# Performance work log

Measured on AMD Instinct MI355X. Metric: run time of the kernel, lower is better.

## Reference

```python
import jax, jax.numpy as jnp
import numpy as np
from jax import lax

B, H, W = 4, 64, 64
D_MODEL, D_INNER, D_STATE, DT_RANK, K = 128, 256, 16, 8, 4


def _ln(x, g, b, eps=1e-5):
    m = x.mean(-1, keepdims=True)
    v = x.var(-1, keepdims=True)
    return (x - m) * lax.rsqrt(v + eps) * g + b


def _conv(x, w, groups=1):
    return lax.conv_general_dilated(x, w, (1, 1), 'SAME', feature_group_count=groups,
                                    dimension_numbers=('NCHW', 'OIHW', 'NCHW'))


def _bn(x, g, b, m, v, eps=1e-5):  # BatchNorm2d eval mode
    s = g * lax.rsqrt(v + eps)
    return x * s[None, :, None, None] + (b - m * s)[None, :, None, None]


def _resblock(x, w1, g1, b1, m1, v1, w2, g2, b2, m2, v2):
    out = jax.nn.relu(_bn(_conv(x, w1), g1, b1, m1, v1))
    out = _bn(_conv(out, w2), g2, b2, m2, v2)
    return jax.nn.relu(out + x)


def _selective_scan(u, delta, A, Bs, Cs, Ds):
    # u, delta: (B,K,D,L); Bs, Cs: (B,K,N,L); A: (K,D,N); Ds: (K,D)
    ins = (jnp.moveaxis(u, -1, 0), jnp.moveaxis(delta, -1, 0),
           jnp.moveaxis(Bs, -1, 0), jnp.moveaxis(Cs, -1, 0))
    h0 = jnp.zeros(u.shape[:3] + (A.shape[-1],), u.dtype)  # (B,K,D,N)
    def step(h, inp):
        u_t, d_t, B_t, C_t = inp
        h = jnp.exp(d_t[..., None] * A) * h + (d_t * u_t)[..., None] * B_t[:, :, None, :]
        return h, jnp.einsum('bkdn,bkn->bkd', h, C_t)
    _, ys = lax.scan(step, h0, ins)
    return jnp.moveaxis(ys, 0, -1) + u * Ds[None, :, :, None]


def _ss2d(x, in_proj_w, dw_w, dw_b, x_proj_w, dt_proj_w, dt_proj_b, A_logs, Ds,
          onorm_g, onorm_b, out_proj_w):
    b, h, w, _ = x.shape
    L = h * w
    xp, z = jnp.split(x @ in_proj_w.T, 2, axis=-1)
    xp = jnp.transpose(xp, (0, 3, 1, 2))  # (B,Dn,H,W)
    xp = jax.nn.silu(_conv(xp, dw_w, groups=D_INNER) + dw_b[None, :, None, None])
    # cross scan: row-major, col-major, and their reverses (K=4)
    x0 = xp.reshape(b, D_INNER, L)
    x1 = jnp.swapaxes(xp, 2, 3).reshape(b, D_INNER, L)
    xs = jnp.stack([x0, x1, x0[..., ::-1], x1[..., ::-1]], axis=1)  # (B,K,Dn,L)
    x_dbl = jnp.einsum('bkdl,kcd->bkcl', xs, x_proj_w)
    dts, Bm, Cm = jnp.split(x_dbl, [DT_RANK, DT_RANK + D_STATE], axis=2)
    delta = jax.nn.softplus(jnp.einsum('bkrl,kdr->bkdl', dts, dt_proj_w)
                            + dt_proj_b[None, :, :, None])
    ys = _selective_scan(xs, delta, -jnp.exp(A_logs), Bm, Cm, Ds)
    # cross merge
    ys = ys[:, 0:2] + ys[:, 2:4][..., ::-1]
    y = ys[:, 0] + jnp.swapaxes(ys[:, 1].reshape(b, D_INNER, w, h), 2, 3).reshape(b, D_INNER, L)
    y = _ln(jnp.transpose(y.reshape(b, D_INNER, h, w), (0, 2, 3, 1)), onorm_g, onorm_b)
    return (y * jax.nn.silu(z)) @ out_proj_w.T


def setup_inputs():
    key = jax.random.key(0)
    ks = iter(jax.random.split(key, 48))
    f32 = jnp.float32
    nrm = lambda shp, s: jax.random.normal(next(ks), shp, f32) * s
    d, dn, n, r = D_MODEL, D_INNER, D_STATE, DT_RANK
    return dict(
        x1=jax.random.normal(next(ks), (B, d, H, W), f32),
        x2=jax.random.normal(next(ks), (B, d, H, W), f32),
        conv_in_w=nrm((d, d), d ** -0.5), conv_in_b=nrm((d,), 0.01),
        ln1_g=jnp.ones(d, f32), ln1_b=jnp.zeros(d, f32),
        in_proj_w=nrm((2 * dn, d), d ** -0.5),
        dw_w=nrm((dn, 1, 3, 3), 1.0 / 3.0), dw_b=nrm((dn,), 0.01),
        x_proj_w=nrm((K, r + 2 * n, dn), dn ** -0.5),
        dt_proj_w=nrm((K, dn, r), r ** -0.5),
        dt_proj_b=jax.random.uniform(next(ks), (K, dn), f32, 0.0, 0.1),
        A_logs=jnp.tile(jnp.log(jnp.arange(1, n + 1, dtype=f32)), (K, dn, 1)),
        Ds=jnp.ones((K, dn), f32),
        onorm_g=jnp.ones(dn, f32), onorm_b=jnp.zeros(dn, f32),
        out_proj_w=nrm((d, dn), dn ** -0.5),
        ln2_g=jnp.ones(d, f32), ln2_b=jnp.zeros(d, f32),
        mlp_w1=nrm((4 * d, d), d ** -0.5), mlp_b1=jnp.zeros(4 * d, f32),
        mlp_w2=nrm((d, 4 * d), (4 * d) ** -0.5), mlp_b2=jnp.zeros(d, f32),
        rb1_w=nrm((d, d, 3, 3), (9 * d) ** -0.5),
        bn1_g=jnp.ones(d, f32), bn1_b=jnp.zeros(d, f32), bn1_m=nrm((d,), 0.1), bn1_v=jnp.ones(d, f32),
        rb2_w=nrm((d, d, 3, 3), (9 * d) ** -0.5),
        bn2_g=jnp.ones(d, f32), bn2_b=jnp.zeros(d, f32), bn2_m=nrm((d,), 0.1), bn2_v=jnp.ones(d, f32),
    )


def reference(x1, x2, conv_in_w, conv_in_b, ln1_g, ln1_b, in_proj_w, dw_w, dw_b,
              x_proj_w, dt_proj_w, dt_proj_b, A_logs, Ds, onorm_g, onorm_b, out_proj_w,
              ln2_g, ln2_b, mlp_w1, mlp_b1, mlp_w2, mlp_b2,
              rb1_w, bn1_g, bn1_b, bn1_m, bn1_v, rb2_w, bn2_g, bn2_b, bn2_m, bn2_v):
    b, c, h, w = x1.shape
    # strided interleave along width: ct[..., ::2]=x1, ct[..., 1::2]=x2
    ct = jnp.stack([x1, x2], axis=-1).reshape(b, c, h, 2 * w)
    x = jnp.einsum('bchw,oc->bohw', ct, conv_in_w) + conv_in_b[None, :, None, None]
    x = jnp.transpose(x, (0, 2, 3, 1))  # (B,H,2W,C) channel-last
    # VSSBlock (drop_path is identity at eval)
    x = x + _ss2d(_ln(x, ln1_g, ln1_b), in_proj_w, dw_w, dw_b, x_proj_w,
                  dt_proj_w, dt_proj_b, A_logs, Ds, onorm_g, onorm_b, out_proj_w)
    hm = _ln(x, ln2_g, ln2_b)
    x = x + (jax.nn.gelu(hm @ mlp_w1.T + mlp_b1, approximate=False) @ mlp_w2.T + mlp_b2)
    xf = jnp.transpose(x, (0, 3, 1, 2))
    x1f = xf[:, :, :, 0::2]
    x2f = xf[:, :, :, 1::2]
    rb = lambda t: _resblock(t, rb1_w, bn1_g, bn1_b, bn1_m, bn1_v,
                             rb2_w, bn2_g, bn2_b, bn2_m, bn2_v)
    return (rb(x1f), rb(x2f))
```

## Files before the change

kernel.cpp:

```cpp
#include <hip/hip_runtime.h>
#include <math.h>

#define BB 4
#define CM 128
#define DI 256
#define NS 16
#define RK 8
#define KD 4
#define HH 64
#define WW 128
#define LL 8192
#define NC 8
#define CH 1024

typedef unsigned short ushortt;
typedef unsigned int uintt;
typedef __attribute__((ext_vector_type(8))) __bf16 bf16x8;
typedef __attribute__((ext_vector_type(4))) float f32x4;

__device__ __forceinline__ void lds_fence(){
  asm volatile("" ::: "memory");
}

__device__ __forceinline__ float sigmoidf_(float x){ return 1.f/(1.f+__expf(-x)); }
__device__ __forceinline__ float siluf_(float x){ return x*sigmoidf_(x); }
__device__ __forceinline__ float softplusf_(float x){
  float r = __logf(1.f + __expf(x));
  return (x > 20.f) ? x : r;
}
__device__ __forceinline__ float geluf_(float x){ return 0.5f*x*(1.f+erff(x*0.70710678118654752f)); }
__device__ __forceinline__ ushortt f2bf(float f){
  uintt u = __float_as_uint(f);
  uintt r = (u + 0x7fffu + ((u>>16)&1u)) >> 16;
  return (ushortt)r;
}
__device__ __forceinline__ float bf2f(ushortt s){
  return __uint_as_float(((uintt)s)<<16);
}
template<int CTRL>
__device__ __forceinline__ float dppadd(float x){
  int r = __builtin_amdgcn_update_dpp(0, __float_as_int(x), CTRL, 0xF, 0xF, true);
  return x + __int_as_float(r);
}
__device__ __forceinline__ float rowsum16(float x){
  x = dppadd<0x121>(x);
  x = dppadd<0x122>(x);
  x = dppadd<0x124>(x);
  x = dppadd<0x128>(x);
  return x;
}
__device__ __forceinline__ float waveReduceSum(float v){
  for (int o=32;o>0;o>>=1) v += __shfl_xor(v,o,64);
  return v;
}

__global__ void k_wall(const float* __restrict__ cw_s, ushortt* __restrict__ cw_d,
                       const float* __restrict__ ip_s, ushortt* __restrict__ ip_d,
                       const float* __restrict__ op_s, ushortt* __restrict__ op_d,
                       const float* __restrict__ m1_s, ushortt* __restrict__ m1_d,
                       const float* __restrict__ m2_s, ushortt* __restrict__ m2_d,
                       const float* __restrict__ r1_s, ushortt* __restrict__ r1_d,
                       const float* __restrict__ r2_s, ushortt* __restrict__ r2_d,
                       const float* __restrict__ dw_s, float* __restrict__ dw_d,
                       const float* __restrict__ xp_s, ushortt* __restrict__ xp_d){
  int i = blockIdx.x*256 + threadIdx.x;
  if (i < 16384){ cw_d[i] = f2bf(cw_s[i]); return; }
  i -= 16384;
  if (i < 65536){ ip_d[i] = f2bf(ip_s[i]); return; }
  i -= 65536;
  if (i < 32768){ op_d[i] = f2bf(op_s[i]); return; }
  i -= 32768;
  if (i < 65536){ m1_d[i] = f2bf(m1_s[i]); return; }
  i -= 65536;
  if (i < 65536){ m2_d[i] = f2bf(m2_s[i]); return; }
  i -= 65536;
  if (i < 147456){ int ci=i&127, co=(i>>7)&127, tap=i>>14;
    r1_d[i]=f2bf(r1_s[(size_t)(co*128+ci)*9+tap]); return; }
  i -= 147456;
  if (i < 147456){ int ci=i&127, co=(i>>7)&127, tap=i>>14;
    r2_d[i]=f2bf(r2_s[(size_t)(co*128+ci)*9+tap]); return; }
  i -= 147456;
  if (i < 2304){ int d = i & 255, tap = i >> 8;
    dw_d[i] = dw_s[d*9 + tap]; return; }
  i -= 2304;
  if (i < 81920){
    int d = i & 255, row = i >> 8;
    float v; int lo;
    if (row < 64){
      int rr = row & 31; int k = rr>>3, c = rr&7;
      v = xp_s[((size_t)(k*40+c))*256 + d];
      lo = (row >= 32);
    } else {
      int rr = row - 64; int q = rr>>6, s = rr&63;
      int j = s & 31;
      v = xp_s[((size_t)(q*40+8+j))*256 + d];
      lo = (s >= 32);
    }
    xp_d[i] = lo ? f2bf(v - bf2f(f2bf(v))) : f2bf(v);
  }
}

__global__ void k_build_ct2(const float* __restrict__ x1, const float* __restrict__ x2,
                            ushortt* __restrict__ CT){
  __shared__ ushortt Tl[64][136];
  int tid = threadIdx.x;
  int p0 = (blockIdx.x & 127) * 64;
  int b  = blockIdx.x >> 7;
  int j = tid & 63;
  int p = p0 + j; int hh = p>>7, ww = p&127, w2 = ww>>1;
  const float* src = (ww&1) ? x2 : x1;
  const float* sp = src + ((size_t)b*128*64 + hh)*64 + w2;
  for (int c0 = tid>>6; c0 < 128; c0 += 4)
    Tl[j][c0] = f2bf(sp[(size_t)c0*4096]);
  __syncthreads();
  int c = tid & 127; int rh = tid >> 7;
  for (int r = rh; r < 64; r += 2)
    CT[((size_t)b*LL + p0 + r)*128 + c] = Tl[r][c];
}

template<int EPI, int NF>
__global__ void k_mgemm(const ushortt* __restrict__ A, const ushortt* __restrict__ W,
                        const float* __restrict__ bias, const float* __restrict__ resid,
                        float* __restrict__ C, ushortt* __restrict__ C2,
                        ushortt* __restrict__ Pp, float* __restrict__ Rp, int N, int K){
  int n0 = blockIdx.x*(NF*16), m0 = blockIdx.y*64;
  int wv = threadIdx.x>>6, l = threadIdx.x&63;
  int ar = l&15, kg = l>>4;
  int mw = m0 + wv*16;
  f32x4 acc[NF];
#pragma unroll
  for (int i=0;i<NF;i++){ acc[i][0]=0.f; acc[i][1]=0.f; acc[i][2]=0.f; acc[i][3]=0.f; }
  const ushortt* Ap = A + (size_t)(mw+ar)*K + kg*8;
  const ushortt* Wp = W + (size_t)(n0+ar)*K + kg*8;
  for (int k0=0; k0<K; k0+=32){
    bf16x8 af = *(const bf16x8*)(Ap + k0);
#pragma unroll
    for (int nf=0; nf<NF; ++nf){
      bf16x8 bfv = *(const bf16x8*)(Wp + (size_t)nf*16*K + k0);
      acc[nf] = __builtin_amdgcn_mfma_f32_16x16x32_bf16(af, bfv, acc[nf], 0,0,0);
    }
  }
#pragma unroll
  for (int nf=0;nf<NF;nf++){
    int n = n0 + nf*16 + ar;
#pragma unroll
    for (int r=0;r<4;r++){
      int m = mw + kg*4 + r;
      float v = acc[nf][r];
      if (EPI==2){
        v += bias[n];
        C2[(size_t)m*512 + n] = f2bf(geluf_(v));
      } else if (EPI==3){
        if (n < 256) Pp[(size_t)m*256 + n] = f2bf(v);
        else         C2[(size_t)m*256 + (n-256)] = f2bf(v);
      } else {
        v += bias[n];
        v += resid[(size_t)m*128 + n];
        int bq = m >> 13; int pq = m & 8191; int yq = pq >> 7; int wq = pq & 127;
        int im = (wq&1)*4 + bq; int xq = wq>>1;
        Pp[(((size_t)im*66 + yq+1)*66 + xq+1)*128 + n] = f2bf(v);
        Rp[(((size_t)im*64 + yq)*64 + xq)*128 + n] = v;
      }
    }
  }
}

template<int RES>
__global__ void k_mgemmln(const ushortt* __restrict__ A, const ushortt* __restrict__ W,
                          const float* __restrict__ bias, float* __restrict__ X,
                          const float* __restrict__ g, const float* __restrict__ bt,
                          ushortt* __restrict__ O, int K){
  int m0 = blockIdx.x*64;
  int wv = threadIdx.x>>6, l = threadIdx.x&63;
  int ar = l&15, kg = l>>4;
  int mw = m0 + wv*16;
  f32x4 acc[8];
#pragma unroll
  for (int i=0;i<8;i++){ acc[i][0]=0.f; acc[i][1]=0.f; acc[i][2]=0.f; acc[i][3]=0.f; }
  const ushortt* Ap = A + (size_t)(mw+ar)*K + kg*8;
  const ushortt* Wp = W + (size_t)ar*K + kg*8;
  for (int k0=0; k0<K; k0+=32){
    bf16x8 af = *(const bf16x8*)(Ap + k0);
#pragma unroll
    for (int nf=0; nf<8; ++nf){
      bf16x8 bfv = *(const bf16x8*)(Wp + (size_t)nf*16*K + k0);
      acc[nf] = __builtin_amdgcn_mfma_f32_16x16x32_bf16(af, bfv, acc[nf], 0,0,0);
    }
  }
  float vv[8][4];
  float s[4] = {0,0,0,0}, s2[4] = {0,0,0,0};
#pragma unroll
  for (int nf=0;nf<8;nf++){
    int n = nf*16 + ar;
    float bv = bias ? bias[n] : 0.f;
#pragma unroll
    for (int r=0;r<4;r++){
      int m = mw + kg*4 + r;
      float v = acc[nf][r] + bv;
      if (RES) v += X[(size_t)m*128 + n];
      X[(size_t)m*128 + n] = v;
      vv[nf][r] = v;
      s[r] += v; s2[r] += v*v;
    }
  }
  float mn[4], rs[4];
#pragma unroll
  for (int r=0;r<4;r++){
    float S  = rowsum16(s[r]);
    float S2 = rowsum16(s2[r]);
    float mean = S*(1.f/128.f);
    float var  = S2*(1.f/128.f) - mean*mean;
    mn[r] = mean; rs[r] = rsqrtf(var + 1e-5f);
  }
#pragma unroll
  for (int nf=0;nf<8;nf++){
    int n = nf*16 + ar;
    float gv = g[n], bv = bt[n];
#pragma unroll
    for (int r=0;r<4;r++){
      int m = mw + kg*4 + r;
      O[(size_t)m*128 + n] = f2bf((vv[nf][r]-mn[r])*rs[r]*gv + bv);
    }
  }
}

__global__ void k_dwconv(const ushortt* __restrict__ Xp, const float* __restrict__ dwt,
                         const float* __restrict__ bias, ushortt* __restrict__ O){
  __shared__ ushortt S[3][18][256];
  int tid = threadIdx.x;
  int ws0 = blockIdx.x*16;
  int hh  = blockIdx.y;
  int b   = blockIdx.z;
  for (int v = tid; v < 1728; v += 256){
    int d0 = (v & 31)*8;
    int r  = v >> 5;
    int dy = r/18, j = r - dy*18;
    int yy = hh + dy - 1, xx = ws0 + j - 1;
    uint4 val = make_uint4(0,0,0,0);
    if (yy>=0 && yy<HH && xx>=0 && xx<WW)
      val = *(const uint4*)(Xp + ((size_t)b*LL + yy*WW + xx)*256 + d0);
    *(uint4*)(&S[dy][j][d0]) = val;
  }
  __syncthreads();
  int d = tid;
  float w[9];
#pragma unroll
  for (int t=0;t<9;t++) w[t] = dwt[t*256+d];
  float bv = bias[d];
  float a0=bf2f(S[0][0][d]), a1=bf2f(S[1][0][d]), a2=bf2f(S[2][0][d]);
  float b0=bf2f(S[0][1][d]), b1=bf2f(S[1][1][d]), b2=bf2f(S[2][1][d]);
  for (int j=0;j<16;j++){
    float c0=bf2f(S[0][j+2][d]), c1=bf2f(S[1][j+2][d]), c2=bf2f(S[2][j+2][d]);
    float acc = bv;
    acc += a0*w[0] + b0*w[1] + c0*w[2];
    acc += a1*w[3] + b1*w[4] + c1*w[5];
    acc += a2*w[6] + b2*w[7] + c2*w[8];
    O[((size_t)b*LL + hh*WW + ws0 + j)*256 + d] = f2bf(siluf_(acc));
    a0=b0; a1=b1; a2=b2; b0=c0; b1=c1; b2=c2;
  }
}

__global__ void k_xtm(const ushortt* __restrict__ Xpab, ushortt* __restrict__ Xpt0,
                      ushortt* __restrict__ Xpt1){
  __shared__ ushortt Tl[64][68];
  int zb = blockIdx.z; int b = zb >> 1; int mode = zb & 1;
  int d0 = blockIdx.y*64;
  int di = threadIdx.x&63, q = threadIdx.x>>6;
  if (mode == 0){
    int p0 = blockIdx.x*64;
    for (int k2=0;k2<16;k2++){ int pi = q*16 + k2;
      Tl[pi][di] = Xpab[((size_t)b*LL + p0+pi)*256 + d0+di]; }
    __syncthreads();
    for (int k2=0;k2<16;k2++){ int dr = q*16 + k2;
      Xpt0[((size_t)(b*256 + d0+dr))*LL + p0+di] = Tl[di][dr]; }
  } else {
    int ww = blockIdx.x;
    for (int k2=0;k2<16;k2++){ int hh = q*16 + k2;
      Tl[hh][di] = Xpab[((size_t)b*LL + hh*128 + ww)*256 + d0+di]; }
    __syncthreads();
    for (int k2=0;k2<16;k2++){ int dr = q*16 + k2;
      Xpt1[((size_t)(b*256 + d0+dr))*LL + ww*64 + di] = Tl[di][dr]; }
  }
}

__global__ void k_xproj(const ushortt* __restrict__ A, const ushortt* __restrict__ W,
                        float* __restrict__ DBCf, char* __restrict__ BCsb){
  int n0 = blockIdx.x*64, m0 = blockIdx.y*64;
  int wv = threadIdx.x>>6, l = threadIdx.x&63;
  int ar = l&15, kg = l>>4;
  int mw = m0 + wv*16;
  f32x4 acc[4];
#pragma unroll
  for (int i=0;i<4;i++){ acc[i][0]=0.f; acc[i][1]=0.f; acc[i][2]=0.f; acc[i][3]=0.f; }
  const ushortt* Ap = A + (size_t)(mw+ar)*256 + kg*8;
  const ushortt* Wp = W + (size_t)(n0+ar)*256 + kg*8;
#pragma unroll
  for (int k0=0; k0<256; k0+=32){
    bf16x8 af = *(const bf16x8*)(Ap + k0);
#pragma unroll
    for (int nf=0; nf<4; ++nf){
      bf16x8 bfv = *(const bf16x8*)(Wp + (size_t)nf*16*256 + k0);
      acc[nf] = __builtin_amdgcn_mfma_f32_16x16x32_bf16(af, bfv, acc[nf], 0,0,0);
    }
  }
  if (blockIdx.x == 0){
#pragma unroll
    for (int nf=0;nf<2;nf++){
      int n = nf*16 + ar;
      int kq = n>>3, cq = n&7;
#pragma unroll
      for (int r=0;r<4;r++){
        int m = mw + kg*4 + r;
        int b = m >> 13, p = m & 8191;
        int hh = p>>7, ww = p&127;
        int tc = (ww<<6)|hh;
        int t = (kq==0)? p : (kq==1)? tc : (kq==2)? (8191-p) : (8191-tc);
        int bk = b*KD + kq;
        DBCf[((size_t)bk*LL + t)*8 + cq] = acc[nf][r] + acc[nf+2][r];
      }
    }
  } else {
    int q = blockIdx.x - 1;
#pragma unroll
    for (int nf=0;nf<2;nf++){
      int st = ar;
      int hi = (nf==1) ? 2 : 0;
#pragma unroll
      for (int r=0;r<4;r++){
        int m = mw + kg*4 + r;
        int b = m >> 13, p = m & 8191;
        int hh = p>>7, ww = p&127;
        int tc = (ww<<6)|hh;
        int t = (q==0)? p : (q==1)? tc : (q==2)? (8191-p) : (8191-tc);
        int bk = b*KD + q;
        float v = acc[nf][r] + acc[nf+2][r];
        size_t a = ((((size_t)bk*512 + (t>>4))*16 + st)*16 + (t&15))*4 + hi;
        *(ushortt*)(BCsb + a) = f2bf(v);
      }
    }
  }
}

__global__ __launch_bounds__(128) void k_scanM(const char* __restrict__ DBCb,
                        const uintt* __restrict__ BCs,
                        const ushortt* __restrict__ Xpt0, const ushortt* __restrict__ Xpt1,
                        const float* __restrict__ dtw_all, const float* __restrict__ dtb_all,
                        const float* __restrict__ A_logs,
                        float* __restrict__ Hbuf, float* __restrict__ Ssum,
                        ushortt* __restrict__ Y0, ushortt* __restrict__ Y1,
                        ushortt* __restrict__ Y2, ushortt* __restrict__ Y3){
  __shared__ float2 sdd[8][16];
  __shared__ float yt[8*328];
  int tid = threadIdx.x;
  int grp = tid >> 4, lane = tid & 15;
  float* ytg = yt + grp*328;
  int gid = blockIdx.x*8 + grp;
  int c = gid & (NC-1);
  int bkd = gid / NC;
  int b = bkd >> 10, k = (bkd>>8)&3, d = bkd & 255;
  int kd = k*256+d;
  int bk = b*KD + k;
  float dtw[8];
  { const float4* w4 = (const float4*)(dtw_all + (size_t)kd*8);
    float4 w0 = w4[0], w1 = w4[1];
    dtw[0]=w0.x; dtw[1]=w0.y; dtw[2]=w0.z; dtw[3]=w0.w;
    dtw[4]=w1.x; dtw[5]=w1.y; dtw[6]=w1.z; dtw[7]=w1.w; }
  float dtb  = dtb_all[kd];
  float Aval = -__expf(A_logs[(size_t)kd*16+lane]);
  const char* dbc = DBCb + (size_t)bk*LL*32;
  const uintt* bcb = BCs + ((size_t)bk*512 + (c*CH>>4))*256;
  const ushortt* Up = ((k&1)?Xpt1:Xpt0) + ((size_t)(b*256+d))*LL;
  ushortt* Yk = (k==0?Y0 : k==1?Y1 : k==2?Y2 : Y3) + ((size_t)b*256 + d)*LL;
  float h = 0.f, Sacc = 0.f;
  int t0 = c*CH;
  const char* row0 = dbc + (size_t)(t0+lane)*32;
  float4 q0 = *(const float4*)row0;
  float4 q1 = *(const float4*)(row0+16);
  ushortt ur = Up[(k<2) ? (t0+lane) : (LL-1-(t0+lane))];
  for (int blk=0; blk<CH/16; ++blk){
    int tb = t0 + blk*16;
    int tme = tb + lane;
    const uint4* bcp = (const uint4*)(bcb + ((size_t)blk*16 + lane)*16);
    uint4 w0 = bcp[0], w1 = bcp[1], w2 = bcp[2], w3 = bcp[3];
    float4 c0 = q0, c1 = q1; ushortt cu = ur;
    if (blk+1 < CH/16){
      const char* rn = dbc + (size_t)(tme+16)*32;
      q0 = *(const float4*)rn;
      q1 = *(const float4*)(rn+16);
      ur = Up[(k<2) ? (tme+16) : (LL-1-(tme+16))];
    }
    float dsum = dtb + c0.x*dtw[0] + c0.y*dtw[1] + c0.z*dtw[2] + c0.w*dtw[3]
                     + c1.x*dtw[4] + c1.y*dtw[5] + c1.z*dtw[6] + c1.w*dtw[7];
    float delta = softplusf_(dsum);
    Sacc += delta;
    float u = bf2f(cu);
    sdd[grp][lane] = make_float2(delta, delta*u);
    lds_fence();
    uintt wd[16] = {w0.x,w0.y,w0.z,w0.w, w1.x,w1.y,w1.z,w1.w,
                    w2.x,w2.y,w2.z,w2.w, w3.x,w3.y,w3.z,w3.w};
#pragma unroll
    for (int i=0;i<16;i++){
      float2 dd = sdd[grp][i];
      uintt w = wd[i];
      float Bn = __uint_as_float(w<<16);
      float Cn = __uint_as_float(w & 0xffff0000u);
      float e = __expf(dd.x * Aval);
      h = e*h + dd.y*Bn;
      ytg[i*20 + lane] = h*Cn;
    }
    lds_fence();
    const f32x4* yr = (const f32x4*)(ytg + lane*20);
    f32x4 s0 = yr[0], s1 = yr[1], s2v = yr[2], s3 = yr[3];
    float acc = (s0[0]+s0[1]+s0[2]+s0[3]) + (s1[0]+s1[1]+s1[2]+s1[3])
              + (s2v[0]+s2v[1]+s2v[2]+s2v[3]) + (s3[0]+s3[1]+s3[2]+s3[3]);
    Yk[tme] = f2bf(acc);
    lds_fence();
  }
  Hbuf[(size_t)gid*16 + lane] = h;
  float Stot = rowsum16(Sacc);
  if (lane==0) Ssum[gid] = Stot;
}

__global__ void k_scanB(const float* __restrict__ Ssum, float* __restrict__ Hbuf,
                        const float* __restrict__ A_logs){
  int idx = blockIdx.x*256 + threadIdx.x;
  int n = idx & 15; int bkd = idx >> 4;
  int kd = ((bkd>>8)&3)*256 + (bkd&255);
  float Aval = -__expf(A_logs[(size_t)kd*16+n]);
  float h = 0.f;
  for (int c=0;c<NC;c++){
    size_t g = (size_t)bkd*NC + c;
    float hout = Hbuf[g*16+n];
    Hbuf[g*16+n] = h;
    h = __expf(Aval*Ssum[g])*h + hout;
  }
}

__global__ __launch_bounds__(128) void k_corr(const char* __restrict__ DBCb,
                       const uintt* __restrict__ BCs,
                       const float* __restrict__ dtw_all, const float* __restrict__ dtb_all,
                       const float* __restrict__ Hbuf,
                       ushortt* __restrict__ Y0, ushortt* __restrict__ Y1,
                       ushortt* __restrict__ Y2, ushortt* __restrict__ Y3){
  int tid = threadIdx.x;
  int grp = tid >> 4, lane = tid & 15;
  int gid = blockIdx.x*8 + grp;
  int c = gid & (NC-1);
  if (c == 0) return;
  int bkd = gid / NC;
  int b = bkd >> 10, k = (bkd>>8)&3, d = bkd & 255;
  int kd = k*256+d;
  int bk = b*KD + k;
  float h0[16];
  float hmax = 0.f;
#pragma unroll
  for (int n=0;n<16;n++){
    h0[n] = Hbuf[(size_t)gid*16 + n];
    hmax = fmaxf(hmax, fabsf(h0[n]));
  }
  float Sexit = 14.f + __logf(fmaxf(hmax, 1e-30f));
  if (0.f > Sexit) return;
  float dtw[8];
  { const float4* w4 = (const float4*)(dtw_all + (size_t)kd*8);
    float4 w0 = w4[0], w1 = w4[1];
    dtw[0]=w0.x; dtw[1]=w0.y; dtw[2]=w0.z; dtw[3]=w0.w;
    dtw[4]=w1.x; dtw[5]=w1.y; dtw[6]=w1.z; dtw[7]=w1.w; }
  float dtb  = dtb_all[kd];
  const char* dbc = DBCb + (size_t)bk*LL*32;
  ushortt* Yk = (k==0?Y0 : k==1?Y1 : k==2?Y2 : Y3) + ((size_t)b*256 + d)*LL;
  float S0 = 0.f;
  int t0 = c*CH;
  for (int blk=0; blk<CH/16; ++blk){
    int tme = t0 + blk*16 + lane;
    const char* rowme = dbc + (size_t)tme*32;
    float4 q0 = *(const float4*)rowme;
    float4 q1 = *(const float4*)(rowme+16);
    float dsum = dtb + q0.x*dtw[0] + q0.y*dtw[1] + q0.z*dtw[2] + q0.w*dtw[3]
                     + q1.x*dtw[4] + q1.y*dtw[5] + q1.z*dtw[6] + q1.w*dtw[7];
    float delta = softplusf_(dsum);
    float pre = delta;
#pragma unroll
    for (int o=1;o<16;o<<=1){
      float t = __shfl_up(pre, o, 16);
      if (lane >= o) pre += t;
    }
    float S = S0 + pre;
    float E = __expf(-S);
    const uintt* cb = BCs + ((size_t)bk*512 + (tme>>4))*256 + (tme&15);
    float p = E, acc = 0.f;
#pragma unroll
    for (int n=0;n<16;n++){
      float Cn = __uint_as_float(cb[n*16] & 0xffff0000u);
      acc += Cn * h0[n] * p;
      p *= E;
    }
    float yv = bf2f(Yk[tme]);
    Yk[tme] = f2bf(yv + acc);
    S0 = __shfl(S, 15, 16);
    if (S0 > Sexit) break;
  }
}

__global__ void k_gate2(const ushortt* __restrict__ Y0, const ushortt* __restrict__ Y1,
                        const ushortt* __restrict__ Y2, const ushortt* __restrict__ Y3,
                        const ushortt* __restrict__ Xpt0, const float* __restrict__ Ds,
                        ushortt* __restrict__ Zg,
                        const float* __restrict__ g, const float* __restrict__ bt){
  __shared__ float ysum[32][257];
  __shared__ float Dl[256];
  int tid = threadIdx.x;
  int wwb = blockIdx.x;
  int hh  = blockIdx.y;
  int b   = blockIdx.z;
  if (tid < 256) Dl[tid] = Ds[tid] + Ds[256+tid] + Ds[512+tid] + Ds[768+tid];
  int ww0 = wwb*32;
  for (int it=0; it<32; ++it){
    int idx = it*256 + tid;
    int d = idx >> 5, tl = idx & 31;
    int ww = ww0 + tl;
    int p  = hh*128 + ww;
    size_t base = ((size_t)b*256 + d) << 13;
    int t1 = ww*64 + hh;
    float v = bf2f(Y0[base + p]) + bf2f(Y2[base + (LL-1) - p])
            + bf2f(Y1[base + t1]) + bf2f(Y3[base + (LL-1) - t1]);
    ysum[tl][d] = v;
  }
  __syncthreads();
  {
    int d = tid;
    if (d < 256){
      size_t ub = (((size_t)b*256 + d) << 13) + hh*128 + ww0;
      const uint4* up = (const uint4*)(Xpt0 + ub);
      uint4 u0 = up[0], u1 = up[1], u2 = up[2], u3 = up[3];
      uintt uw[16] = {u0.x,u0.y,u0.z,u0.w, u1.x,u1.y,u1.z,u1.w,
                      u2.x,u2.y,u2.z,u2.w, u3.x,u3.y,u3.z,u3.w};
      float Dd = Dl[d];
#pragma unroll
      for (int qd=0; qd<16; ++qd){
        float ulo = __uint_as_float(uw[qd]<<16);
        float uhi = __uint_as_float(uw[qd] & 0xffff0000u);
        ysum[2*qd][d]   += Dd*ulo;
        ysum[2*qd+1][d] += Dd*uhi;
      }
    }
  }
  __syncthreads();
  int wave = tid >> 6, lane = tid & 63;
  for (int tk = wave*8; tk < wave*8+8; ++tk){
    float v0 = ysum[tk][lane], v1 = ysum[tk][lane+64];
    float v2 = ysum[tk][lane+128], v3 = ysum[tk][lane+192];
    float s  = waveReduceSum(v0+v1+v2+v3);
    float s2 = waveReduceSum(v0*v0+v1*v1+v2*v2+v3*v3);
    float mean = s*(1.f/256.f);
    float var  = s2*(1.f/256.f) - mean*mean;
    float r = rsqrtf(var + 1e-5f);
    int p = hh*128 + ww0 + tk;
    size_t zb = (((size_t)b<<13) + p) << 8;
#pragma unroll
    for (int j=0;j<4;j++){
      int dd = lane + 64*j;
      float ln = (ysum[tk][dd]-mean)*r*g[dd] + bt[dd];
      float z = bf2f(Zg[zb + dd]);
      Zg[zb + dd] = f2bf(ln * siluf_(z));
    }
  }
}

template<int FINAL>
__global__ void k_mconv(const ushortt* __restrict__ I, const ushortt* __restrict__ Wt,
                        const float* __restrict__ g, const float* __restrict__ bb,
                        const float* __restrict__ mn, const float* __restrict__ vv,
                        const float* __restrict__ R, ushortt* __restrict__ Op,
                        float* __restrict__ Of){
  int y  = blockIdx.x;
  int im = blockIdx.y;
  int wv = threadIdx.x>>6, l = threadIdx.x&63;
  int ar = l&15, kg = l>>4;
  int x0 = wv*16;
  f32x4 acc[8];
#pragma unroll
  for (int i=0;i<8;i++){ acc[i][0]=0.f; acc[i][1]=0.f; acc[i][2]=0.f; acc[i][3]=0.f; }
  const ushortt* Ibase = I + (((size_t)im*66 + y)*66 + x0 + ar)*128 + kg*8;
  const ushortt* Wbase = Wt + (size_t)ar*128 + kg*8;
#pragma unroll
  for (int tap=0; tap<9; ++tap){
    int dy = tap/3, dx = tap - dy*3;
    const ushortt* Ir = Ibase + ((size_t)dy*66 + dx)*128;
    const ushortt* Wr = Wbase + (size_t)tap*16384;
#pragma unroll
    for (int kc=0;kc<4;kc++){
      bf16x8 af = *(const bf16x8*)(Ir + kc*32);
#pragma unroll
      for (int nf=0;nf<8;nf++){
        bf16x8 bfv = *(const bf16x8*)(Wr + (size_t)nf*16*128 + kc*32);
        acc[nf] = __builtin_amdgcn_mfma_f32_16x16x32_bf16(af, bfv, acc[nf], 0,0,0);
      }
    }
  }
#pragma unroll
  for (int nf=0;nf<8;nf++){
    int co = nf*16 + ar;
    float s  = g[co]*rsqrtf(vv[co]+1e-5f);
    float sh = bb[co] - mn[co]*s;
#pragma unroll
    for (int r=0;r<4;r++){
      int x = x0 + kg*4 + r;
      float v = acc[nf][r]*s + sh;
      if (FINAL){
        v += R[(((size_t)im*64 + y)*64 + x)*128 + co];
        v = fmaxf(v, 0.f);
        Of[(((size_t)im*128 + co)*64 + y)*64 + x] = v;
      } else {
        v = fmaxf(v, 0.f);
        Op[(((size_t)im*66 + (y+1))*66 + (x+1))*128 + co] = f2bf(v);
      }
    }
  }
}

extern "C" void kernel_launch(void* const* d_in, const int* in_sizes, int n_in,
                              void* d_out, int out_size, void* d_ws, size_t ws_size,
                              hipStream_t stream){
  const float* x1        = (const float*)d_in[0];
  const float* x2        = (const float*)d_in[1];
  const float* conv_in_w = (const float*)d_in[2];
  const float* conv_in_b = (const float*)d_in[3];
  const float* ln1_g     = (const float*)d_in[4];
  const float* ln1_b     = (const float*)d_in[5];
  const float* in_proj_w = (const float*)d_in[6];
  const float* dw_w      = (const float*)d_in[7];
  const float* dw_b      = (const float*)d_in[8];
  const float* x_proj_w  = (const float*)d_in[9];
  const float* dt_proj_w = (const float*)d_in[10];
  const float* dt_proj_b = (const float*)d_in[11];
  const float* A_logs    = (const float*)d_in[12];
  const float* Ds        = (const float*)d_in[13];
  const float* onorm_g   = (const float*)d_in[14];
  const float* onorm_b   = (const float*)d_in[15];
  const float* out_proj_w= (const float*)d_in[16];
  const float* ln2_g     = (const float*)d_in[17];
  const float* ln2_b     = (const float*)d_in[18];
  const float* mlp_w1    = (const float*)d_in[19];
  const float* mlp_b1    = (const float*)d_in[20];
  const float* mlp_w2    = (const float*)d_in[21];
  const float* mlp_b2    = (const float*)d_in[22];
  const float* rb1_w     = (const float*)d_in[23];
  const float* bn1_g     = (const float*)d_in[24];
  const float* bn1_b     = (const float*)d_in[25];
  const float* bn1_m     = (const float*)d_in[26];
  const float* bn1_v     = (const float*)d_in[27];
  const float* rb2_w     = (const float*)d_in[28];
  const float* bn2_g     = (const float*)d_in[29];
  const float* bn2_b     = (const float*)d_in[30];
  const float* bn2_m     = (const float*)d_in[31];
  const float* bn2_v     = (const float*)d_in[32];

  float* ws = (float*)d_ws;
  char*  wsB = (char*)d_ws;
  const size_t FM = 262144;
  const size_t MB = 1048576;
  float*   X0   = ws;
  ushortt* Xpab = (ushortt*)(wsB + 16*MB);
  ushortt* Xpt0 = (ushortt*)(wsB + 32*MB);
  ushortt* Xpt1 = (ushortt*)(wsB + 48*MB);
  char*    DBCb = wsB + 64*MB;
  uintt*   BCs  = (uintt*)(wsB + 68*MB);
  ushortt* Zg   = (ushortt*)(wsB + 77*MB);
  ushortt* Y0   = (ushortt*)(wsB + 93*MB);
  ushortt* Y1   = (ushortt*)(wsB + 109*MB);
  ushortt* Y2   = (ushortt*)(wsB + 125*MB);
  ushortt* Y3   = Xpab;
  float*   Hbuf = ws + 141*FM;
  float*   Ssum = ws + 145*FM;
  ushortt* CT   = (ushortt*)(wsB + 93*MB);
  ushortt* Lnb  = (ushortt*)(wsB + 101*MB);
  ushortt* Xpb  = (ushortt*)(wsB + 109*MB);
  ushortt* Ln2b = (ushortt*)(wsB + 93*MB);
  ushortt* H1   = (ushortt*)(wsB + 109*MB);
  ushortt* P    = (ushortt*)(wsB + 16*MB);
  ushortt* T    = (ushortt*)(wsB + 25*MB);
  float*   R    = (float*)(wsB + 34*MB);
  ushortt* cw  = (ushortt*)(wsB + 146*MB);
  ushortt* ipw = (ushortt*)(wsB + 146*MB + 32*1024);
  ushortt* opw = (ushortt*)(wsB + 146*MB + 160*1024);
  ushortt* m1w = (ushortt*)(wsB + 146*MB + 224*1024);
  ushortt* m2w = (ushortt*)(wsB + 146*MB + 352*1024);
  ushortt* rw1 = (ushortt*)(wsB + 146*MB + 480*1024);
  ushortt* rw2 = (ushortt*)(wsB + 146*MB + 768*1024);
  ushortt* xpw = (ushortt*)(wsB + 146*MB + 1056*1024);
  float*   dwt = (float*)(wsB + 146*MB + 1216*1024);
  float* out = (float*)d_out;

  k_wall<<<2441,256,0,stream>>>(conv_in_w,cw, in_proj_w,ipw, out_proj_w,opw,
                                mlp_w1,m1w, mlp_w2,m2w, rb1_w,rw1, rb2_w,rw2,
                                dw_w, dwt, x_proj_w, xpw);
  k_build_ct2<<<512,256,0,stream>>>(x1,x2,CT);
  k_mgemmln<0><<<512,256,0,stream>>>(CT, cw, conv_in_b, X0, ln1_g, ln1_b, Lnb, 128);
  k_mgemm<3,16><<<dim3(2,512),256,0,stream>>>(Lnb, ipw, nullptr, nullptr, nullptr, Zg, Xpb, nullptr, 512,128);
  k_dwconv<<<dim3(8,64,BB),256,0,stream>>>(Xpb, dwt, dw_b, Xpab);
  k_xtm<<<dim3(128,4,2*BB),256,0,stream>>>(Xpab, Xpt0, Xpt1);
  k_xproj<<<dim3(5,512),256,0,stream>>>(Xpab, xpw, (float*)DBCb, (char*)BCs);
  k_scanM<<<4096,128,0,stream>>>(DBCb, BCs, Xpt0, Xpt1, dt_proj_w, dt_proj_b, A_logs,
                                 Hbuf, Ssum, Y0,Y1,Y2,Y3);
  k_scanB<<<256,256,0,stream>>>(Ssum, Hbuf, A_logs);
  k_corr<<<4096,128,0,stream>>>(DBCb, BCs, dt_proj_w, dt_proj_b, Hbuf, Y0,Y1,Y2,Y3);
  k_gate2<<<dim3(4,64,BB),256,0,stream>>>(Y0,Y1,Y2,Y3, Xpt0, Ds, Zg, onorm_g, onorm_b);
  k_mgemmln<1><<<512,256,0,stream>>>(Zg, opw, nullptr, X0, ln2_g, ln2_b, Ln2b, 256);
  hipMemsetAsync(wsB + 16*MB, 0, 18*MB, stream);
  k_mgemm<2,16><<<dim3(2,512),256,0,stream>>>(Ln2b, m1w, mlp_b1, nullptr, nullptr, H1, nullptr,nullptr, 512,128);
  k_mgemm<4,8><<<dim3(1,512),256,0,stream>>>(H1, m2w, mlp_b2, X0, nullptr, nullptr, P, R, 128,512);
  k_mconv<0><<<dim3(64,8),256,0,stream>>>(P, rw1, bn1_g,bn1_b,bn1_m,bn1_v, nullptr, T, nullptr);
  k_mconv<1><<<dim3(64,8),256,0,stream>>>(T, rw2, bn2_g,bn2_b,bn2_m,bn2_v, R, nullptr, out);
}
```

Measured before the change: 724.6 us.

## Fuse row-major transpose into dwconv and chunk-carry combine into k_corr

```diff
diff --git a/kernel.cpp b/kernel.cpp
--- a/kernel.cpp
+++ b/kernel.cpp
@@ -225,7 +225,8 @@
 }
 
 __global__ void k_dwconv(const ushortt* __restrict__ Xp, const float* __restrict__ dwt,
-                         const float* __restrict__ bias, ushortt* __restrict__ O){
+                         const float* __restrict__ bias, ushortt* __restrict__ O,
+                         ushortt* __restrict__ Xpt0){
   __shared__ ushortt S[3][18][256];
   int tid = threadIdx.x;
   int ws0 = blockIdx.x*16;
@@ -247,6 +248,7 @@
 #pragma unroll
   for (int t=0;t<9;t++) w[t] = dwt[t*256+d];
   float bv = bias[d];
+  ushortt outs[16];
   float a0=bf2f(S[0][0][d]), a1=bf2f(S[1][0][d]), a2=bf2f(S[2][0][d]);
   float b0=bf2f(S[0][1][d]), b1=bf2f(S[1][1][d]), b2=bf2f(S[2][1][d]);
   for (int j=0;j<16;j++){
@@ -255,32 +257,30 @@
     acc += a0*w[0] + b0*w[1] + c0*w[2];
     acc += a1*w[3] + b1*w[4] + c1*w[5];
     acc += a2*w[6] + b2*w[7] + c2*w[8];
-    O[((size_t)b*LL + hh*WW + ws0 + j)*256 + d] = f2bf(siluf_(acc));
+    ushortt ov = f2bf(siluf_(acc));
+    outs[j] = ov;
+    O[((size_t)b*LL + hh*WW + ws0 + j)*256 + d] = ov;
     a0=b0; a1=b1; a2=b2; b0=c0; b1=c1; b2=c2;
   }
-}
-
-__global__ void k_xtm(const ushortt* __restrict__ Xpab, ushortt* __restrict__ Xpt0,
-                      ushortt* __restrict__ Xpt1){
+  uintt pk[8];
+#pragma unroll
+  for (int q=0;q<8;q++) pk[q] = (uintt)outs[2*q] | ((uintt)outs[2*q+1]<<16);
+  ushortt* dst = Xpt0 + ((size_t)(b*256+d))*LL + hh*WW + ws0;
+  *(uint4*)dst       = make_uint4(pk[0],pk[1],pk[2],pk[3]);
+  *(uint4*)(dst + 8) = make_uint4(pk[4],pk[5],pk[6],pk[7]);
+}
+
+__global__ void k_xtm(const ushortt* __restrict__ Xpab, ushortt* __restrict__ Xpt1){
   __shared__ ushortt Tl[64][68];
-  int zb = blockIdx.z; int b = zb >> 1; int mode = zb & 1;
+  int b = blockIdx.z;
   int d0 = blockIdx.y*64;
+  int ww = blockIdx.x;
   int di = threadIdx.x&63, q = threadIdx.x>>6;
-  if (mode == 0){
-    int p0 = blockIdx.x*64;
-    for (int k2=0;k2<16;k2++){ int pi = q*16 + k2;
-      Tl[pi][di] = Xpab[((size_t)b*LL + p0+pi)*256 + d0+di]; }
-    __syncthreads();
-    for (int k2=0;k2<16;k2++){ int dr = q*16 + k2;
-      Xpt0[((size_t)(b*256 + d0+dr))*LL + p0+di] = Tl[di][dr]; }
-  } else {
-    int ww = blockIdx.x;
-    for (int k2=0;k2<16;k2++){ int hh = q*16 + k2;
-      Tl[hh][di] = Xpab[((size_t)b*LL + hh*128 + ww)*256 + d0+di]; }
-    __syncthreads();
-    for (int k2=0;k2<16;k2++){ int dr = q*16 + k2;
-      Xpt1[((size_t)(b*256 + d0+dr))*LL + ww*64 + di] = Tl[di][dr]; }
-  }
+  for (int k2=0;k2<16;k2++){ int hh = q*16 + k2;
+    Tl[hh][di] = Xpab[((size_t)b*LL + hh*128 + ww)*256 + d0+di]; }
+  __syncthreads();
+  for (int k2=0;k2<16;k2++){ int dr = q*16 + k2;
+    Xpt1[((size_t)(b*256 + d0+dr))*LL + ww*64 + di] = Tl[di][dr]; }
 }
 
 __global__ void k_xproj(const ushortt* __restrict__ A, const ushortt* __restrict__ W,
@@ -421,27 +421,14 @@
   if (lane==0) Ssum[gid] = Stot;
 }
 
-__global__ void k_scanB(const float* __restrict__ Ssum, float* __restrict__ Hbuf,
-                        const float* __restrict__ A_logs){
-  int idx = blockIdx.x*256 + threadIdx.x;
-  int n = idx & 15; int bkd = idx >> 4;
-  int kd = ((bkd>>8)&3)*256 + (bkd&255);
-  float Aval = -__expf(A_logs[(size_t)kd*16+n]);
-  float h = 0.f;
-  for (int c=0;c<NC;c++){
-    size_t g = (size_t)bkd*NC + c;
-    float hout = Hbuf[g*16+n];
-    Hbuf[g*16+n] = h;
-    h = __expf(Aval*Ssum[g])*h + hout;
-  }
-}
-
 __global__ __launch_bounds__(128) void k_corr(const char* __restrict__ DBCb,
                        const uintt* __restrict__ BCs,
                        const float* __restrict__ dtw_all, const float* __restrict__ dtb_all,
-                       const float* __restrict__ Hbuf,
+                       const float* __restrict__ A_logs,
+                       const float* __restrict__ Hbuf, const float* __restrict__ Ssum,
                        ushortt* __restrict__ Y0, ushortt* __restrict__ Y1,
                        ushortt* __restrict__ Y2, ushortt* __restrict__ Y3){
+  __shared__ float hs[8][16];
   int tid = threadIdx.x;
   int grp = tid >> 4, lane = tid & 15;
   int gid = blockIdx.x*8 + grp;
@@ -451,11 +438,21 @@
   int b = bkd >> 10, k = (bkd>>8)&3, d = bkd & 255;
   int kd = k*256+d;
   int bk = b*KD + k;
+  {
+    float Avn = -__expf(A_logs[(size_t)kd*16+lane]);
+    float h = 0.f;
+    for (int j=0; j<c; ++j){
+      size_t gj = (size_t)bkd*NC + j;
+      h = __expf(Avn*Ssum[gj])*h + Hbuf[gj*16 + lane];
+    }
+    hs[grp][lane] = h;
+  }
+  lds_fence();
   float h0[16];
   float hmax = 0.f;
 #pragma unroll
   for (int n=0;n<16;n++){
-    h0[n] = Hbuf[(size_t)gid*16 + n];
+    h0[n] = hs[grp][n];
     hmax = fmaxf(hmax, fabsf(h0[n]));
   }
   float Sexit = 14.f + __logf(fmaxf(hmax, 1e-30f));
@@ -697,13 +694,13 @@
   k_build_ct2<<<512,256,0,stream>>>(x1,x2,CT);
   k_mgemmln<0><<<512,256,0,stream>>>(CT, cw, conv_in_b, X0, ln1_g, ln1_b, Lnb, 128);
   k_mgemm<3,16><<<dim3(2,512),256,0,stream>>>(Lnb, ipw, nullptr, nullptr, nullptr, Zg, Xpb, nullptr, 512,128);
-  k_dwconv<<<dim3(8,64,BB),256,0,stream>>>(Xpb, dwt, dw_b, Xpab);
-  k_xtm<<<dim3(128,4,2*BB),256,0,stream>>>(Xpab, Xpt0, Xpt1);
+  k_dwconv<<<dim3(8,64,BB),256,0,stream>>>(Xpb, dwt, dw_b, Xpab, Xpt0);
+  k_xtm<<<dim3(128,4,BB),256,0,stream>>>(Xpab, Xpt1);
   k_xproj<<<dim3(5,512),256,0,stream>>>(Xpab, xpw, (float*)DBCb, (char*)BCs);
   k_scanM<<<4096,128,0,stream>>>(DBCb, BCs, Xpt0, Xpt1, dt_proj_w, dt_proj_b, A_logs,
                                  Hbuf, Ssum, Y0,Y1,Y2,Y3);
-  k_scanB<<<256,256,0,stream>>>(Ssum, Hbuf, A_logs);
-  k_corr<<<4096,128,0,stream>>>(DBCb, BCs, dt_proj_w, dt_proj_b, Hbuf, Y0,Y1,Y2,Y3);
+  k_corr<<<4096,128,0,stream>>>(DBCb, BCs, dt_proj_w, dt_proj_b, A_logs, Hbuf, Ssum,
+                                Y0,Y1,Y2,Y3);
   k_gate2<<<dim3(4,64,BB),256,0,stream>>>(Y0,Y1,Y2,Y3, Xpt0, Ds, Zg, onorm_g, onorm_b);
   k_mgemmln<1><<<512,256,0,stream>>>(Zg, opw, nullptr, X0, ln2_g, ln2_b, Ln2b, 256);
   hipMemsetAsync(wsB + 16*MB, 0, 18*MB, stream);
```

After: 722.2 us. Within noise of the previous version (-0.3%).
